# Kernel tuning notes

Hardware: AMD Instinct MI355X
Metric: run time of the kernel (lower is better)

Reference implementation:

```python
import jax, jax.numpy as jnp
import numpy as np

N = 50000
E = 600000
D = 128


def setup_inputs() -> dict:
    key = jax.random.key(0)
    ks = jax.random.split(key, 10)
    scale = 1.0 / np.sqrt(D)
    inp = {
        "x": jax.random.normal(ks[0], (N, D), dtype=jnp.float32),
        "edge_index": jax.random.randint(ks[1], (2, E), 0, N, dtype=jnp.int64),
        # layer 0: fc + res_fc (residual=True, activation=relu)
        "W1": jax.random.normal(ks[2], (D, D), dtype=jnp.float32) * scale,
        "R1": jax.random.normal(ks[3], (D, D), dtype=jnp.float32) * scale,
        # layer 1
        "W2": jax.random.normal(ks[4], (D, D), dtype=jnp.float32) * scale,
        "R2": jax.random.normal(ks[5], (D, D), dtype=jnp.float32) * scale,
        # layer 2 (last, encoding=False -> no residual/activation)
        "W3": jax.random.normal(ks[6], (D, D), dtype=jnp.float32) * scale,
        # head Linear(out_dim, out_dim) with bias
        "Wh": jax.random.normal(ks[7], (D, D), dtype=jnp.float32) * scale,
        "bh": jnp.zeros((D,), dtype=jnp.float32),
    }
    return inp


def _gcn_stack(x, row, col, norm, W1, R1, W2, R2, W3, Wh, bh):
    n = x.shape[0]

    def conv(x, W, R, act):
        h = x @ W                                   # [N, D]
        msg = h[row] * norm[:, None]                # gather + per-edge scale [E+N, D]
        agg = jax.ops.segment_sum(msg, col, num_segments=n)  # scatter-add [N, D]
        if R is not None:
            agg = agg + x @ R                       # residual
        if act:
            agg = jax.nn.relu(agg)
        return agg

    x = conv(x, W1, R1, True)
    x = conv(x, W2, R2, True)
    x = conv(x, W3, None, False)
    return x @ Wh + bh


def reference(x, edge_index, W1, R1, W2, R2, W3, Wh, bh):
    n = x.shape[0]
    # add self loops (same edge structure for every layer)
    loops = jnp.arange(n, dtype=edge_index.dtype)
    row = jnp.concatenate([edge_index[0], loops])
    col = jnp.concatenate([edge_index[1], loops])
    # symmetric degree normalization: deg computed over col (incl. self loops)
    deg = jax.ops.segment_sum(jnp.ones_like(col, dtype=x.dtype), col, num_segments=n)
    dinv = deg ** -0.5
    norm = dinv[row] * dinv[col]                    # [E+N]
    return _gcn_stack(x, row, col, norm, W1, R1, W2, R2, W3, Wh, bh)
```

## Files before the change

kernel.cpp:

```cpp
#include <hip/hip_runtime.h>
#include <hip/hip_bf16.h>


#define SCAN_CHUNK 1024

typedef _Float16 half8 __attribute__((ext_vector_type(8)));
typedef _Float16 half4 __attribute__((ext_vector_type(4)));
typedef float floatx4 __attribute__((ext_vector_type(4)));

__global__ void zero_int_kernel(int* __restrict__ p, int n) {
    int i = blockIdx.x * blockDim.x + threadIdx.x;
    if (i < n) p[i] = 0;
}

__global__ void hist_kernel(const int* __restrict__ col, int* __restrict__ cnt, int E) {
    int i = blockIdx.x * blockDim.x + threadIdx.x;
    if (i < E) atomicAdd(&cnt[col[i]], 1);
}

__global__ __launch_bounds__(256) void scan_reduce_kernel(
        const int* __restrict__ cnt, int* __restrict__ bsum, int n) {
    __shared__ int s[256];
    int b = blockIdx.x, t = threadIdx.x;
    int base = b * SCAN_CHUNK + t * 4;
    int v = 0;
    if (base + 3 < n) {
        int4 q = *(const int4*)&cnt[base];
        v = q.x + q.y + q.z + q.w;
    } else {
        for (int i = 0; i < 4; ++i) if (base + i < n) v += cnt[base + i];
    }
    s[t] = v;
    __syncthreads();
    for (int off = 128; off > 0; off >>= 1) {
        if (t < off) s[t] += s[t + off];
        __syncthreads();
    }
    if (t == 0) bsum[b] = s[0];
}

__global__ __launch_bounds__(1024) void scan_bsum_kernel(
        const int* __restrict__ bsum, int* __restrict__ boff, int nb) {
    __shared__ int s[1024];
    int t = threadIdx.x;
    s[t] = (t < nb) ? bsum[t] : 0;
    __syncthreads();
    for (int off = 1; off < 1024; off <<= 1) {
        int add = (t >= off) ? s[t - off] : 0;
        __syncthreads();
        s[t] += add;
        __syncthreads();
    }
    if (t < nb) boff[t] = (t == 0) ? 0 : s[t - 1];
}

__global__ __launch_bounds__(256) void scan_write_kernel(
        const int* __restrict__ cnt, const int* __restrict__ boff,
        int* __restrict__ row_ptr, int* __restrict__ cursor,
        float* __restrict__ dinv, int n, int E) {
    __shared__ int s[256];
    int b = blockIdx.x, t = threadIdx.x;
    int base = b * SCAN_CHUNK + t * 4;
    int v[4];
    int sum = 0;
    for (int i = 0; i < 4; ++i) {
        v[i] = (base + i < n) ? cnt[base + i] : 0;
        sum += v[i];
    }
    s[t] = sum;
    __syncthreads();
    for (int off = 1; off < 256; off <<= 1) {
        int add = (t >= off) ? s[t - off] : 0;
        __syncthreads();
        s[t] += add;
        __syncthreads();
    }
    int prefix = boff[b] + ((t == 0) ? 0 : s[t - 1]);
    for (int i = 0; i < 4; ++i) {
        if (base + i < n) {
            row_ptr[base + i] = prefix;
            cursor[base + i] = prefix;
            dinv[base + i] = rsqrtf((float)(v[i] + 1));
            prefix += v[i];
        }
    }
    if (b == 0 && t == 0) row_ptr[n] = E;
}

__global__ void fill_kernel(const int* __restrict__ row, const int* __restrict__ colv,
                            const float* __restrict__ dinv, int* __restrict__ cursor,
                            unsigned* __restrict__ csr, int E) {
    int i = blockIdx.x * blockDim.x + threadIdx.x;
    if (i < E) {
        int r = row[i], c = colv[i];
        int p = atomicAdd(&cursor[c], 1);
        _Float16 nrm = (_Float16)(dinv[r] * dinv[c]);
        unsigned hn = (unsigned)__builtin_bit_cast(unsigned short, nrm);
        csr[p] = (unsigned)r | (hn << 16);
    }
}

__global__ __launch_bounds__(256) void wcvt_wc_kernel(
        const float* __restrict__ W1, const float* __restrict__ R1,
        const float* __restrict__ W2, const float* __restrict__ R2,
        const float* __restrict__ W3, const float* __restrict__ Wh,
        _Float16* __restrict__ Wt) {
    int b = blockIdx.x;
    int t = threadIdx.x;
    if (b < 64) {
        __shared__ float tile[32][33];
        int mat = b >> 4, tl = b & 15;
        const float* W = (mat == 0) ? W1 : (mat == 1) ? R1 : (mat == 2) ? W2 : R2;
        _Float16* T = Wt + (size_t)mat * 16384;
        int tr = (tl >> 2) * 32, tc = (tl & 3) * 32;
        int i = t >> 3, j4 = t & 7;
        float4 v = *(const float4*)&W[(tr + i) * 128 + tc + j4 * 4];
        tile[i][j4 * 4 + 0] = v.x;
        tile[i][j4 * 4 + 1] = v.y;
        tile[i][j4 * 4 + 2] = v.z;
        tile[i][j4 * 4 + 3] = v.w;
        __syncthreads();
        half4 h;
        h.x = (_Float16)tile[j4 * 4 + 0][i];
        h.y = (_Float16)tile[j4 * 4 + 1][i];
        h.z = (_Float16)tile[j4 * 4 + 2][i];
        h.w = (_Float16)tile[j4 * 4 + 3][i];
        *(half4*)&T[(tc + i) * 128 + tr + j4 * 4] = h;
    } else {
        int bb = b - 64;
        _Float16* Wtc = Wt + (size_t)4 * 16384;
        int c = bb * 8 + (t >> 5);
        int k0 = (t & 31) * 4;
        float acc0 = 0.f, acc1 = 0.f, acc2 = 0.f, acc3 = 0.f;
        for (int j = 0; j < 128; ++j) {
            float wh = Wh[j * 128 + c];
            acc0 = fmaf(W3[(k0 + 0) * 128 + j], wh, acc0);
            acc1 = fmaf(W3[(k0 + 1) * 128 + j], wh, acc1);
            acc2 = fmaf(W3[(k0 + 2) * 128 + j], wh, acc2);
            acc3 = fmaf(W3[(k0 + 3) * 128 + j], wh, acc3);
        }
        half4 h;
        h.x = (_Float16)acc0; h.y = (_Float16)acc1;
        h.z = (_Float16)acc2; h.w = (_Float16)acc3;
        *(half4*)&Wtc[c * 128 + k0] = h;
    }
}

template <int F32IN>
__global__ __launch_bounds__(256) void gemm_dual_kernel(
        const void* __restrict__ Xv, const _Float16* __restrict__ WtA,
        const _Float16* __restrict__ WtB, _Float16* __restrict__ outA,
        _Float16* __restrict__ outB, int n) {
    __shared__ _Float16 Af[64 * 136];
    __shared__ _Float16 Bt[128 * 136];
    int t = threadIdx.x;
    int r0 = blockIdx.x * 64;

    if (F32IN) {
        const float* X = (const float*)Xv;
#pragma unroll
        for (int i = 0; i < 8; ++i) {
            int flat = i * 256 + t;
            int r = flat >> 5, c4 = flat & 31;
            float4 v = make_float4(0.f, 0.f, 0.f, 0.f);
            if (r0 + r < n) v = ((const float4*)X)[(size_t)(r0 + r) * 32 + c4];
            half4 h;
            h.x = (_Float16)v.x; h.y = (_Float16)v.y;
            h.z = (_Float16)v.z; h.w = (_Float16)v.w;
            *(half4*)&Af[r * 136 + c4 * 4] = h;
        }
    } else {
        const _Float16* X = (const _Float16*)Xv;
#pragma unroll
        for (int i = 0; i < 4; ++i) {
            int flat = i * 256 + t;
            int r = flat >> 4, k8 = flat & 15;
            half8 v = {0, 0, 0, 0, 0, 0, 0, 0};
            if (r0 + r < n) v = *(const half8*)&X[(size_t)(r0 + r) * 128 + k8 * 8];
            *(half8*)&Af[r * 136 + k8 * 8] = v;
        }
    }
#pragma unroll
    for (int i = 0; i < 8; ++i) {
        int flat = i * 256 + t;
        int c = flat >> 4, k8 = flat & 15;
        *(half8*)&Bt[c * 136 + k8 * 8] = *(const half8*)&WtA[c * 128 + k8 * 8];
    }
    __syncthreads();

    int lane = t & 63, w = t >> 6;
    int m = lane & 15, q = lane >> 4;
    int rowb = r0 + w * 16 + q * 4;

    half8 a[4];
#pragma unroll
    for (int s = 0; s < 4; ++s)
        a[s] = *(const half8*)&Af[(w * 16 + m) * 136 + s * 32 + q * 8];

    floatx4 acc[8];
#pragma unroll
    for (int nt = 0; nt < 8; ++nt) acc[nt] = (floatx4){0.f, 0.f, 0.f, 0.f};
#pragma unroll
    for (int s = 0; s < 4; ++s)
#pragma unroll
        for (int nt = 0; nt < 8; ++nt) {
            half8 b = *(const half8*)&Bt[(nt * 16 + m) * 136 + s * 32 + q * 8];
            acc[nt] = __builtin_amdgcn_mfma_f32_16x16x32_f16(a[s], b, acc[nt], 0, 0, 0);
        }
    __syncthreads();
#pragma unroll
    for (int i = 0; i < 8; ++i) {
        int flat = i * 256 + t;
        int c = flat >> 4, k8 = flat & 15;
        *(half8*)&Bt[c * 136 + k8 * 8] = *(const half8*)&WtB[c * 128 + k8 * 8];
    }
#pragma unroll
    for (int nt = 0; nt < 8; ++nt) {
        int col = nt * 16 + m;
#pragma unroll
        for (int r = 0; r < 4; ++r) {
            int gr = rowb + r;
            if (gr < n) outA[(size_t)gr * 128 + col] = (_Float16)acc[nt][r];
        }
    }
    __syncthreads();

#pragma unroll
    for (int nt = 0; nt < 8; ++nt) acc[nt] = (floatx4){0.f, 0.f, 0.f, 0.f};
#pragma unroll
    for (int s = 0; s < 4; ++s)
#pragma unroll
        for (int nt = 0; nt < 8; ++nt) {
            half8 b = *(const half8*)&Bt[(nt * 16 + m) * 136 + s * 32 + q * 8];
            acc[nt] = __builtin_amdgcn_mfma_f32_16x16x32_f16(a[s], b, acc[nt], 0, 0, 0);
        }
#pragma unroll
    for (int nt = 0; nt < 8; ++nt) {
        int col = nt * 16 + m;
#pragma unroll
        for (int r = 0; r < 4; ++r) {
            int gr = rowb + r;
            if (gr < n) outB[(size_t)gr * 128 + col] = (_Float16)acc[nt][r];
        }
    }
}

__global__ __launch_bounds__(256) void gemm_h_kernel(
        const _Float16* __restrict__ X, const _Float16* __restrict__ Wt,
        _Float16* __restrict__ out, int n) {
    __shared__ _Float16 Af[64 * 136];
    __shared__ _Float16 Bt[128 * 136];
    int t = threadIdx.x;
    int r0 = blockIdx.x * 64;

#pragma unroll
    for (int i = 0; i < 4; ++i) {
        int flat = i * 256 + t;
        int r = flat >> 4, k8 = flat & 15;
        half8 v = {0, 0, 0, 0, 0, 0, 0, 0};
        if (r0 + r < n) v = *(const half8*)&X[(size_t)(r0 + r) * 128 + k8 * 8];
        *(half8*)&Af[r * 136 + k8 * 8] = v;
    }
#pragma unroll
    for (int i = 0; i < 8; ++i) {
        int flat = i * 256 + t;
        int c = flat >> 4, k8 = flat & 15;
        *(half8*)&Bt[c * 136 + k8 * 8] = *(const half8*)&Wt[c * 128 + k8 * 8];
    }
    __syncthreads();

    int lane = t & 63, w = t >> 6;
    int m = lane & 15, q = lane >> 4;

    floatx4 acc[8];
#pragma unroll
    for (int nt = 0; nt < 8; ++nt) acc[nt] = (floatx4){0.f, 0.f, 0.f, 0.f};

#pragma unroll
    for (int s = 0; s < 4; ++s) {
        half8 a = *(const half8*)&Af[(w * 16 + m) * 136 + s * 32 + q * 8];
#pragma unroll
        for (int nt = 0; nt < 8; ++nt) {
            half8 b = *(const half8*)&Bt[(nt * 16 + m) * 136 + s * 32 + q * 8];
            acc[nt] = __builtin_amdgcn_mfma_f32_16x16x32_f16(a, b, acc[nt], 0, 0, 0);
        }
    }

    int rowb = r0 + w * 16 + q * 4;
#pragma unroll
    for (int nt = 0; nt < 8; ++nt) {
        int col = nt * 16 + m;
#pragma unroll
        for (int r = 0; r < 4; ++r) {
            int gr = rowb + r;
            if (gr < n) out[(size_t)gr * 128 + col] = (_Float16)acc[nt][r];
        }
    }
}

template <int RELU, int FINAL>
__global__ void spmm_kernel(const _Float16* __restrict__ h, const _Float16* __restrict__ xr,
                            const int* __restrict__ row_ptr, const unsigned* __restrict__ csr,
                            const float* __restrict__ dinv, _Float16* __restrict__ outh,
                            float* __restrict__ outf, const float* __restrict__ bias,
                            int n) {
    int gid = blockIdx.x * blockDim.x + threadIdx.x;
    int node = gid >> 4;
    int fl = gid & 15;
    if (node >= n) return;
    const half8* hp8 = (const half8*)h;

    float acc[8];
#pragma unroll
    for (int j = 0; j < 8; ++j) acc[j] = 0.f;

    int e0 = row_ptr[node], e1 = row_ptr[node + 1];
    for (int e = e0; e < e1; e += 4) {
        int i1 = e + 1, i2 = e + 2, i3 = e + 3;
        int a1 = i1 < e1, a2 = i2 < e1, a3 = i3 < e1;
        unsigned d0 = csr[e];
        unsigned d1 = csr[a1 ? i1 : e];
        unsigned d2 = csr[a2 ? i2 : e];
        unsigned d3 = csr[a3 ? i3 : e];
        half8 v0 = hp8[(size_t)(d0 & 0xffffu) * 16 + fl];
        half8 v1 = hp8[(size_t)(d1 & 0xffffu) * 16 + fl];
        half8 v2 = hp8[(size_t)(d2 & 0xffffu) * 16 + fl];
        half8 v3 = hp8[(size_t)(d3 & 0xffffu) * 16 + fl];
        float n0 = (float)__builtin_bit_cast(_Float16, (unsigned short)(d0 >> 16));
        float n1 = a1 ? (float)__builtin_bit_cast(_Float16, (unsigned short)(d1 >> 16)) : 0.f;
        float n2 = a2 ? (float)__builtin_bit_cast(_Float16, (unsigned short)(d2 >> 16)) : 0.f;
        float n3 = a3 ? (float)__builtin_bit_cast(_Float16, (unsigned short)(d3 >> 16)) : 0.f;
#pragma unroll
        for (int j = 0; j < 8; ++j) {
            acc[j] = fmaf(n0, (float)v0[j], acc[j]);
            acc[j] = fmaf(n1, (float)v1[j], acc[j]);
            acc[j] = fmaf(n2, (float)v2[j], acc[j]);
            acc[j] = fmaf(n3, (float)v3[j], acc[j]);
        }
    }

    float di = dinv[node];
    float w = di * di;
    half8 hv = hp8[(size_t)node * 16 + fl];
#pragma unroll
    for (int j = 0; j < 8; ++j) acc[j] = fmaf(w, (float)hv[j], acc[j]);
    if (!FINAL && xr) {
        half8 r = ((const half8*)xr)[(size_t)node * 16 + fl];
#pragma unroll
        for (int j = 0; j < 8; ++j) acc[j] += (float)r[j];
    }
    if (RELU) {
#pragma unroll
        for (int j = 0; j < 8; ++j) acc[j] = fmaxf(acc[j], 0.f);
    }
    if (FINAL) {
        float4 b0 = *(const float4*)&bias[fl * 8];
        float4 b1 = *(const float4*)&bias[fl * 8 + 4];
        float4 o0 = make_float4(acc[0] + b0.x, acc[1] + b0.y,
                                acc[2] + b0.z, acc[3] + b0.w);
        float4 o1 = make_float4(acc[4] + b1.x, acc[5] + b1.y,
                                acc[6] + b1.z, acc[7] + b1.w);
        ((float4*)outf)[(size_t)node * 32 + fl * 2] = o0;
        ((float4*)outf)[(size_t)node * 32 + fl * 2 + 1] = o1;
    } else {
        half8 o;
#pragma unroll
        for (int j = 0; j < 8; ++j) o[j] = (_Float16)acc[j];
        ((half8*)outh)[(size_t)node * 16 + fl] = o;
    }
}

extern "C" void kernel_launch(void* const* d_in, const int* in_sizes, int n_in,
                              void* d_out, int out_size, void* d_ws, size_t ws_size,
                              hipStream_t stream) {
    const float* x  = (const float*)d_in[0];
    const int*   ei = (const int*)d_in[1];
    const float* W1 = (const float*)d_in[2];
    const float* R1 = (const float*)d_in[3];
    const float* W2 = (const float*)d_in[4];
    const float* R2 = (const float*)d_in[5];
    const float* W3 = (const float*)d_in[6];
    const float* Wh = (const float*)d_in[7];
    const float* bh = (const float*)d_in[8];
    float* out = (float*)d_out;

    int N = in_sizes[0] / 128;
    int E = in_sizes[1] / 2;

    char* p = (char*)d_ws;
    auto alloc = [&](size_t bytes) {
        char* r = p;
        p += (bytes + 255) & ~(size_t)255;
        return r;
    };
    int*      cnt     = (int*)alloc((size_t)N * 4);
    int*      row_ptr = (int*)alloc((size_t)(N + 1) * 4);
    int*      cursor  = (int*)alloc((size_t)N * 4);
    float*    dinv    = (float*)alloc((size_t)N * 4);
    int*      bsum    = (int*)alloc((size_t)1024 * 4);
    int*      boff    = (int*)alloc((size_t)1024 * 4);
    unsigned* csr     = (unsigned*)alloc((size_t)E * 4);
    _Float16* Wt      = (_Float16*)alloc((size_t)5 * 16384 * 2);
    _Float16* B0h     = (_Float16*)alloc((size_t)N * 128 * 2);
    _Float16* B1h     = (_Float16*)alloc((size_t)N * 128 * 2);
    _Float16* B2h     = (_Float16*)alloc((size_t)N * 128 * 2);

    const int* rowi = ei;
    const int* coli = ei + E;

    int nb = (N + SCAN_CHUNK - 1) / SCAN_CHUNK;

    zero_int_kernel<<<(N + 255) / 256, 256, 0, stream>>>(cnt, N);
    hist_kernel<<<(E + 255) / 256, 256, 0, stream>>>(coli, cnt, E);
    scan_reduce_kernel<<<nb, 256, 0, stream>>>(cnt, bsum, N);
    scan_bsum_kernel<<<1, 1024, 0, stream>>>(bsum, boff, nb);
    scan_write_kernel<<<nb, 256, 0, stream>>>(cnt, boff, row_ptr, cursor, dinv, N, E);
    fill_kernel<<<(E + 255) / 256, 256, 0, stream>>>(rowi, coli, dinv, cursor, csr, E);
    wcvt_wc_kernel<<<80, 256, 0, stream>>>(W1, R1, W2, R2, W3, Wh, Wt);

    int gb = (N + 63) / 64;
    int sb = ((size_t)N * 16 + 255) / 256;
    _Float16* Wt1 = Wt;
    _Float16* Rt1 = Wt + 16384;
    _Float16* Wt2 = Wt + 2 * 16384;
    _Float16* Rt2 = Wt + 3 * 16384;
    _Float16* Wtc = Wt + 4 * 16384;

    gemm_dual_kernel<1><<<gb, 256, 0, stream>>>(x, Wt1, Rt1, B0h, B1h, N);
    spmm_kernel<1, 0><<<sb, 256, 0, stream>>>(B0h, B1h, row_ptr, csr, dinv,
                                              B1h, nullptr, nullptr, N);
    gemm_dual_kernel<0><<<gb, 256, 0, stream>>>(B1h, Wt2, Rt2, B0h, B2h, N);
    spmm_kernel<1, 0><<<sb, 256, 0, stream>>>(B0h, B2h, row_ptr, csr, dinv,
                                              B2h, nullptr, nullptr, N);
    gemm_h_kernel<<<gb, 256, 0, stream>>>(B2h, Wtc, B0h, N);
    spmm_kernel<0, 1><<<sb, 256, 0, stream>>>(B0h, nullptr, row_ptr, csr, dinv,
                                              nullptr, out, bh, N);
}
```

Before: 296.3 us.

## Fuse SpMM aggregation into following GEMM and merge prep kernels

Each layer's sparse aggregation (gather, scale, residual, ReLU) now runs inside the next layer's GEMM kernel. The aggregated fp16 rows go straight into shared memory as the MFMA A-tile instead of making a round trip through global memory, which removes two kernel launches and the write and re-read of intermediate feature matrices. The counter-zeroing and weight-conversion kernels are also merged into one launch. In exchange, the fused kernel does the irregular gather with only 64 rows per block, so load balance and occupancy may be worse than the standalone SpMM, and an extra buffer is allocated.

After: 299.4 us. Within noise of the previous version (+1.1%).

```diff
diff --git a/kernel.cpp b/kernel.cpp
--- a/kernel.cpp
+++ b/kernel.cpp
@@ -8,9 +8,57 @@
 typedef _Float16 half4 __attribute__((ext_vector_type(4)));
 typedef float floatx4 __attribute__((ext_vector_type(4)));
 
-__global__ void zero_int_kernel(int* __restrict__ p, int n) {
-    int i = blockIdx.x * blockDim.x + threadIdx.x;
-    if (i < n) p[i] = 0;
+__global__ __launch_bounds__(256) void prep0_kernel(
+        int* __restrict__ cnt, int n, int nzb,
+        const float* __restrict__ W1, const float* __restrict__ R1,
+        const float* __restrict__ W2, const float* __restrict__ R2,
+        const float* __restrict__ W3, const float* __restrict__ Wh,
+        _Float16* __restrict__ Wt) {
+    int b = blockIdx.x;
+    int t = threadIdx.x;
+    if (b < nzb) {
+        int i = b * 256 + t;
+        if (i < n) cnt[i] = 0;
+        return;
+    }
+    int b2 = b - nzb;
+    if (b2 < 64) {
+        __shared__ float tile[32][33];
+        int mat = b2 >> 4, tl = b2 & 15;
+        const float* W = (mat == 0) ? W1 : (mat == 1) ? R1 : (mat == 2) ? W2 : R2;
+        _Float16* T = Wt + (size_t)mat * 16384;
+        int tr = (tl >> 2) * 32, tc = (tl & 3) * 32;
+        int i = t >> 3, j4 = t & 7;
+        float4 v = *(const float4*)&W[(tr + i) * 128 + tc + j4 * 4];
+        tile[i][j4 * 4 + 0] = v.x;
+        tile[i][j4 * 4 + 1] = v.y;
+        tile[i][j4 * 4 + 2] = v.z;
+        tile[i][j4 * 4 + 3] = v.w;
+        __syncthreads();
+        half4 h;
+        h.x = (_Float16)tile[j4 * 4 + 0][i];
+        h.y = (_Float16)tile[j4 * 4 + 1][i];
+        h.z = (_Float16)tile[j4 * 4 + 2][i];
+        h.w = (_Float16)tile[j4 * 4 + 3][i];
+        *(half4*)&T[(tc + i) * 128 + tr + j4 * 4] = h;
+    } else {
+        int bb = b2 - 64;
+        _Float16* Wtc = Wt + (size_t)4 * 16384;
+        int c = bb * 8 + (t >> 5);
+        int k0 = (t & 31) * 4;
+        float acc0 = 0.f, acc1 = 0.f, acc2 = 0.f, acc3 = 0.f;
+        for (int j = 0; j < 128; ++j) {
+            float wh = Wh[j * 128 + c];
+            acc0 = fmaf(W3[(k0 + 0) * 128 + j], wh, acc0);
+            acc1 = fmaf(W3[(k0 + 1) * 128 + j], wh, acc1);
+            acc2 = fmaf(W3[(k0 + 2) * 128 + j], wh, acc2);
+            acc3 = fmaf(W3[(k0 + 3) * 128 + j], wh, acc3);
+        }
+        half4 h;
+        h.x = (_Float16)acc0; h.y = (_Float16)acc1;
+        h.z = (_Float16)acc2; h.w = (_Float16)acc3;
+        *(half4*)&Wtc[c * 128 + k0] = h;
+    }
 }
 
 __global__ void hist_kernel(const int* __restrict__ col, int* __restrict__ cnt, int E) {
@@ -100,55 +148,8 @@
     }
 }
 
-__global__ __launch_bounds__(256) void wcvt_wc_kernel(
-        const float* __restrict__ W1, const float* __restrict__ R1,
-        const float* __restrict__ W2, const float* __restrict__ R2,
-        const float* __restrict__ W3, const float* __restrict__ Wh,
-        _Float16* __restrict__ Wt) {
-    int b = blockIdx.x;
-    int t = threadIdx.x;
-    if (b < 64) {
-        __shared__ float tile[32][33];
-        int mat = b >> 4, tl = b & 15;
-        const float* W = (mat == 0) ? W1 : (mat == 1) ? R1 : (mat == 2) ? W2 : R2;
-        _Float16* T = Wt + (size_t)mat * 16384;
-        int tr = (tl >> 2) * 32, tc = (tl & 3) * 32;
-        int i = t >> 3, j4 = t & 7;
-        float4 v = *(const float4*)&W[(tr + i) * 128 + tc + j4 * 4];
-        tile[i][j4 * 4 + 0] = v.x;
-        tile[i][j4 * 4 + 1] = v.y;
-        tile[i][j4 * 4 + 2] = v.z;
-        tile[i][j4 * 4 + 3] = v.w;
-        __syncthreads();
-        half4 h;
-        h.x = (_Float16)tile[j4 * 4 + 0][i];
-        h.y = (_Float16)tile[j4 * 4 + 1][i];
-        h.z = (_Float16)tile[j4 * 4 + 2][i];
-        h.w = (_Float16)tile[j4 * 4 + 3][i];
-        *(half4*)&T[(tc + i) * 128 + tr + j4 * 4] = h;
-    } else {
-        int bb = b - 64;
-        _Float16* Wtc = Wt + (size_t)4 * 16384;
-        int c = bb * 8 + (t >> 5);
-        int k0 = (t & 31) * 4;
-        float acc0 = 0.f, acc1 = 0.f, acc2 = 0.f, acc3 = 0.f;
-        for (int j = 0; j < 128; ++j) {
-            float wh = Wh[j * 128 + c];
-            acc0 = fmaf(W3[(k0 + 0) * 128 + j], wh, acc0);
-            acc1 = fmaf(W3[(k0 + 1) * 128 + j], wh, acc1);
-            acc2 = fmaf(W3[(k0 + 2) * 128 + j], wh, acc2);
-            acc3 = fmaf(W3[(k0 + 3) * 128 + j], wh, acc3);
-        }
-        half4 h;
-        h.x = (_Float16)acc0; h.y = (_Float16)acc1;
-        h.z = (_Float16)acc2; h.w = (_Float16)acc3;
-        *(half4*)&Wtc[c * 128 + k0] = h;
-    }
-}
-
-template <int F32IN>
-__global__ __launch_bounds__(256) void gemm_dual_kernel(
-        const void* __restrict__ Xv, const _Float16* __restrict__ WtA,
+__global__ __launch_bounds__(256) void gemm_dual_f32_kernel(
+        const float* __restrict__ X, const _Float16* __restrict__ WtA,
         const _Float16* __restrict__ WtB, _Float16* __restrict__ outA,
         _Float16* __restrict__ outB, int n) {
     __shared__ _Float16 Af[64 * 136];
@@ -156,29 +157,16 @@
     int t = threadIdx.x;
     int r0 = blockIdx.x * 64;
 
-    if (F32IN) {
-        const float* X = (const float*)Xv;
-#pragma unroll
-        for (int i = 0; i < 8; ++i) {
-            int flat = i * 256 + t;
-            int r = flat >> 5, c4 = flat & 31;
-            float4 v = make_float4(0.f, 0.f, 0.f, 0.f);
-            if (r0 + r < n) v = ((const float4*)X)[(size_t)(r0 + r) * 32 + c4];
-            half4 h;
-            h.x = (_Float16)v.x; h.y = (_Float16)v.y;
-            h.z = (_Float16)v.z; h.w = (_Float16)v.w;
-            *(half4*)&Af[r * 136 + c4 * 4] = h;
-        }
-    } else {
-        const _Float16* X = (const _Float16*)Xv;
-#pragma unroll
-        for (int i = 0; i < 4; ++i) {
-            int flat = i * 256 + t;
-            int r = flat >> 4, k8 = flat & 15;
-            half8 v = {0, 0, 0, 0, 0, 0, 0, 0};
-            if (r0 + r < n) v = *(const half8*)&X[(size_t)(r0 + r) * 128 + k8 * 8];
-            *(half8*)&Af[r * 136 + k8 * 8] = v;
-        }
+#pragma unroll
+    for (int i = 0; i < 8; ++i) {
+        int flat = i * 256 + t;
+        int r = flat >> 5, c4 = flat & 31;
+        float4 v = make_float4(0.f, 0.f, 0.f, 0.f);
+        if (r0 + r < n) v = ((const float4*)X)[(size_t)(r0 + r) * 32 + c4];
+        half4 h;
+        h.x = (_Float16)v.x; h.y = (_Float16)v.y;
+        h.z = (_Float16)v.z; h.w = (_Float16)v.w;
+        *(half4*)&Af[r * 136 + c4 * 4] = h;
     }
 #pragma unroll
     for (int i = 0; i < 8; ++i) {
@@ -245,65 +233,144 @@
     }
 }
 
-__global__ __launch_bounds__(256) void gemm_h_kernel(
-        const _Float16* __restrict__ X, const _Float16* __restrict__ Wt,
-        _Float16* __restrict__ out, int n) {
+template <int DUAL>
+__global__ __launch_bounds__(256) void spmm_gemm_kernel(
+        const _Float16* __restrict__ h, const _Float16* __restrict__ xr,
+        const int* __restrict__ row_ptr, const unsigned* __restrict__ csr,
+        const float* __restrict__ dinv,
+        const _Float16* __restrict__ WtA, const _Float16* __restrict__ WtB,
+        _Float16* __restrict__ outA, _Float16* __restrict__ outB, int n) {
     __shared__ _Float16 Af[64 * 136];
     __shared__ _Float16 Bt[128 * 136];
     int t = threadIdx.x;
     int r0 = blockIdx.x * 64;
-
-#pragma unroll
-    for (int i = 0; i < 4; ++i) {
-        int flat = i * 256 + t;
-        int r = flat >> 4, k8 = flat & 15;
-        half8 v = {0, 0, 0, 0, 0, 0, 0, 0};
-        if (r0 + r < n) v = *(const half8*)&X[(size_t)(r0 + r) * 128 + k8 * 8];
-        *(half8*)&Af[r * 136 + k8 * 8] = v;
-    }
+    const half8* hp8 = (const half8*)h;
+
 #pragma unroll
     for (int i = 0; i < 8; ++i) {
         int flat = i * 256 + t;
         int c = flat >> 4, k8 = flat & 15;
-        *(half8*)&Bt[c * 136 + k8 * 8] = *(const half8*)&Wt[c * 128 + k8 * 8];
+        *(half8*)&Bt[c * 136 + k8 * 8] = *(const half8*)&WtA[c * 128 + k8 * 8];
+    }
+
+    int fl = t & 15;
+#pragma unroll
+    for (int it = 0; it < 4; ++it) {
+        int lr = it * 16 + (t >> 4);
+        int node = r0 + lr;
+        float acc[8];
+#pragma unroll
+        for (int j = 0; j < 8; ++j) acc[j] = 0.f;
+        if (node < n) {
+            int e0 = row_ptr[node], e1 = row_ptr[node + 1];
+            for (int e = e0; e < e1; e += 4) {
+                int i1 = e + 1, i2 = e + 2, i3 = e + 3;
+                int a1 = i1 < e1, a2 = i2 < e1, a3 = i3 < e1;
+                unsigned d0 = csr[e];
+                unsigned d1 = csr[a1 ? i1 : e];
+                unsigned d2 = csr[a2 ? i2 : e];
+                unsigned d3 = csr[a3 ? i3 : e];
+                half8 v0 = hp8[(size_t)(d0 & 0xffffu) * 16 + fl];
+                half8 v1 = hp8[(size_t)(d1 & 0xffffu) * 16 + fl];
+                half8 v2 = hp8[(size_t)(d2 & 0xffffu) * 16 + fl];
+                half8 v3 = hp8[(size_t)(d3 & 0xffffu) * 16 + fl];
+                float n0 = (float)__builtin_bit_cast(_Float16, (unsigned short)(d0 >> 16));
+                float n1 = a1 ? (float)__builtin_bit_cast(_Float16, (unsigned short)(d1 >> 16)) : 0.f;
+                float n2 = a2 ? (float)__builtin_bit_cast(_Float16, (unsigned short)(d2 >> 16)) : 0.f;
+                float n3 = a3 ? (float)__builtin_bit_cast(_Float16, (unsigned short)(d3 >> 16)) : 0.f;
+#pragma unroll
+                for (int j = 0; j < 8; ++j) {
+                    acc[j] = fmaf(n0, (float)v0[j], acc[j]);
+                    acc[j] = fmaf(n1, (float)v1[j], acc[j]);
+                    acc[j] = fmaf(n2, (float)v2[j], acc[j]);
+                    acc[j] = fmaf(n3, (float)v3[j], acc[j]);
+                }
+            }
+            float di = dinv[node];
+            float w = di * di;
+            half8 hv = hp8[(size_t)node * 16 + fl];
+            half8 r = ((const half8*)xr)[(size_t)node * 16 + fl];
+#pragma unroll
+            for (int j = 0; j < 8; ++j) {
+                acc[j] = fmaf(w, (float)hv[j], acc[j]);
+                acc[j] += (float)r[j];
+                acc[j] = fmaxf(acc[j], 0.f);
+            }
+        }
+        half8 o;
+#pragma unroll
+        for (int j = 0; j < 8; ++j) o[j] = (_Float16)acc[j];
+        *(half8*)&Af[lr * 136 + fl * 8] = o;
     }
     __syncthreads();
 
     int lane = t & 63, w = t >> 6;
     int m = lane & 15, q = lane >> 4;
+    int rowb = r0 + w * 16 + q * 4;
+
+    half8 a[4];
+#pragma unroll
+    for (int s = 0; s < 4; ++s)
+        a[s] = *(const half8*)&Af[(w * 16 + m) * 136 + s * 32 + q * 8];
 
     floatx4 acc[8];
 #pragma unroll
     for (int nt = 0; nt < 8; ++nt) acc[nt] = (floatx4){0.f, 0.f, 0.f, 0.f};
-
-#pragma unroll
-    for (int s = 0; s < 4; ++s) {
-        half8 a = *(const half8*)&Af[(w * 16 + m) * 136 + s * 32 + q * 8];
+#pragma unroll
+    for (int s = 0; s < 4; ++s)
 #pragma unroll
         for (int nt = 0; nt < 8; ++nt) {
             half8 b = *(const half8*)&Bt[(nt * 16 + m) * 136 + s * 32 + q * 8];
-            acc[nt] = __builtin_amdgcn_mfma_f32_16x16x32_f16(a, b, acc[nt], 0, 0, 0);
-        }
-    }
-
-    int rowb = r0 + w * 16 + q * 4;
+            acc[nt] = __builtin_amdgcn_mfma_f32_16x16x32_f16(a[s], b, acc[nt], 0, 0, 0);
+        }
+
+    if (DUAL) {
+        __syncthreads();
+#pragma unroll
+        for (int i = 0; i < 8; ++i) {
+            int flat = i * 256 + t;
+            int c = flat >> 4, k8 = flat & 15;
+            *(half8*)&Bt[c * 136 + k8 * 8] = *(const half8*)&WtB[c * 128 + k8 * 8];
+        }
+    }
 #pragma unroll
     for (int nt = 0; nt < 8; ++nt) {
         int col = nt * 16 + m;
 #pragma unroll
         for (int r = 0; r < 4; ++r) {
             int gr = rowb + r;
-            if (gr < n) out[(size_t)gr * 128 + col] = (_Float16)acc[nt][r];
-        }
-    }
-}
-
-template <int RELU, int FINAL>
-__global__ void spmm_kernel(const _Float16* __restrict__ h, const _Float16* __restrict__ xr,
-                            const int* __restrict__ row_ptr, const unsigned* __restrict__ csr,
-                            const float* __restrict__ dinv, _Float16* __restrict__ outh,
-                            float* __restrict__ outf, const float* __restrict__ bias,
-                            int n) {
+            if (gr < n) outA[(size_t)gr * 128 + col] = (_Float16)acc[nt][r];
+        }
+    }
+    if (DUAL) {
+        __syncthreads();
+#pragma unroll
+        for (int nt = 0; nt < 8; ++nt) acc[nt] = (floatx4){0.f, 0.f, 0.f, 0.f};
+#pragma unroll
+        for (int s = 0; s < 4; ++s)
+#pragma unroll
+            for (int nt = 0; nt < 8; ++nt) {
+                half8 b = *(const half8*)&Bt[(nt * 16 + m) * 136 + s * 32 + q * 8];
+                acc[nt] = __builtin_amdgcn_mfma_f32_16x16x32_f16(a[s], b, acc[nt], 0, 0, 0);
+            }
+#pragma unroll
+        for (int nt = 0; nt < 8; ++nt) {
+            int col = nt * 16 + m;
+#pragma unroll
+            for (int r = 0; r < 4; ++r) {
+                int gr = rowb + r;
+                if (gr < n) outB[(size_t)gr * 128 + col] = (_Float16)acc[nt][r];
+            }
+        }
+    }
+}
+
+__global__ void spmm_final_kernel(const _Float16* __restrict__ h,
+                                  const int* __restrict__ row_ptr,
+                                  const unsigned* __restrict__ csr,
+                                  const float* __restrict__ dinv,
+                                  float* __restrict__ outf,
+                                  const float* __restrict__ bias, int n) {
     int gid = blockIdx.x * blockDim.x + threadIdx.x;
     int node = gid >> 4;
     int fl = gid & 15;
@@ -344,30 +411,15 @@
     half8 hv = hp8[(size_t)node * 16 + fl];
 #pragma unroll
     for (int j = 0; j < 8; ++j) acc[j] = fmaf(w, (float)hv[j], acc[j]);
-    if (!FINAL && xr) {
-        half8 r = ((const half8*)xr)[(size_t)node * 16 + fl];
-#pragma unroll
-        for (int j = 0; j < 8; ++j) acc[j] += (float)r[j];
-    }
-    if (RELU) {
-#pragma unroll
-        for (int j = 0; j < 8; ++j) acc[j] = fmaxf(acc[j], 0.f);
-    }
-    if (FINAL) {
-        float4 b0 = *(const float4*)&bias[fl * 8];
-        float4 b1 = *(const float4*)&bias[fl * 8 + 4];
-        float4 o0 = make_float4(acc[0] + b0.x, acc[1] + b0.y,
-                                acc[2] + b0.z, acc[3] + b0.w);
-        float4 o1 = make_float4(acc[4] + b1.x, acc[5] + b1.y,
-                                acc[6] + b1.z, acc[7] + b1.w);
-        ((float4*)outf)[(size_t)node * 32 + fl * 2] = o0;
-        ((float4*)outf)[(size_t)node * 32 + fl * 2 + 1] = o1;
-    } else {
-        half8 o;
-#pragma unroll
-        for (int j = 0; j < 8; ++j) o[j] = (_Float16)acc[j];
-        ((half8*)outh)[(size_t)node * 16 + fl] = o;
-    }
+
+    float4 b0 = *(const float4*)&bias[fl * 8];
+    float4 b1 = *(const float4*)&bias[fl * 8 + 4];
+    float4 o0 = make_float4(acc[0] + b0.x, acc[1] + b0.y,
+                            acc[2] + b0.z, acc[3] + b0.w);
+    float4 o1 = make_float4(acc[4] + b1.x, acc[5] + b1.y,
+                            acc[6] + b1.z, acc[7] + b1.w);
+    ((float4*)outf)[(size_t)node * 32 + fl * 2] = o0;
+    ((float4*)outf)[(size_t)node * 32 + fl * 2 + 1] = o1;
 }
 
 extern "C" void kernel_launch(void* const* d_in, const int* in_sizes, int n_in,
@@ -404,19 +456,20 @@
     _Float16* B0h     = (_Float16*)alloc((size_t)N * 128 * 2);
     _Float16* B1h     = (_Float16*)alloc((size_t)N * 128 * 2);
     _Float16* B2h     = (_Float16*)alloc((size_t)N * 128 * 2);
+    _Float16* B3h     = (_Float16*)alloc((size_t)N * 128 * 2);
 
     const int* rowi = ei;
     const int* coli = ei + E;
 
     int nb = (N + SCAN_CHUNK - 1) / SCAN_CHUNK;
-
-    zero_int_kernel<<<(N + 255) / 256, 256, 0, stream>>>(cnt, N);
+    int nzb = (N + 255) / 256;
+
+    prep0_kernel<<<nzb + 80, 256, 0, stream>>>(cnt, N, nzb, W1, R1, W2, R2, W3, Wh, Wt);
     hist_kernel<<<(E + 255) / 256, 256, 0, stream>>>(coli, cnt, E);
     scan_reduce_kernel<<<nb, 256, 0, stream>>>(cnt, bsum, N);
     scan_bsum_kernel<<<1, 1024, 0, stream>>>(bsum, boff, nb);
     scan_write_kernel<<<nb, 256, 0, stream>>>(cnt, boff, row_ptr, cursor, dinv, N, E);
     fill_kernel<<<(E + 255) / 256, 256, 0, stream>>>(rowi, coli, dinv, cursor, csr, E);
-    wcvt_wc_kernel<<<80, 256, 0, stream>>>(W1, R1, W2, R2, W3, Wh, Wt);
 
     int gb = (N + 63) / 64;
     int sb = ((size_t)N * 16 + 255) / 256;
@@ -426,13 +479,10 @@
     _Float16* Rt2 = Wt + 3 * 16384;
     _Float16* Wtc = Wt + 4 * 16384;
 
-    gemm_dual_kernel<1><<<gb, 256, 0, stream>>>(x, Wt1, Rt1, B0h, B1h, N);
-    spmm_kernel<1, 0><<<sb, 256, 0, stream>>>(B0h, B1h, row_ptr, csr, dinv,
-                                              B1h, nullptr, nullptr, N);
-    gemm_dual_kernel<0><<<gb, 256, 0, stream>>>(B1h, Wt2, Rt2, B0h, B2h, N);
-    spmm_kernel<1, 0><<<sb, 256, 0, stream>>>(B0h, B2h, row_ptr, csr, dinv,
-                                              B2h, nullptr, nullptr, N);
-    gemm_h_kernel<<<gb, 256, 0, stream>>>(B2h, Wtc, B0h, N);
-    spmm_kernel<0, 1><<<sb, 256, 0, stream>>>(B0h, nullptr, row_ptr, csr, dinv,
-                                              nullptr, out, bh, N);
-}
+    gemm_dual_f32_kernel<<<gb, 256, 0, stream>>>(x, Wt1, Rt1, B0h, B1h, N);
+    spmm_gemm_kernel<1><<<gb, 256, 0, stream>>>(B0h, B1h, row_ptr, csr, dinv,
+                                                Wt2, Rt2, B3h, B2h, N);
+    spmm_gemm_kernel<0><<<gb, 256, 0, stream>>>(B3h, B2h, row_ptr, csr, dinv,
+                                                Wtc, nullptr, B0h, nullptr, N);
+    spmm_final_kernel<<<sb, 256, 0, stream>>>(B0h, row_ptr, csr, dinv, out, bh, N);
+}
```
